# Kernel optimization log

Measured on AMD Instinct MI355X. Metric: run time of the kernel, lower is better.

The kernel has to match this reference:

```python
import jax, jax.numpy as jnp
import numpy as np

N = 100000
E = 1000000
N_FEAT = 128
N_HID = 16
N_HEAD = 8
HIDDEN = N_HID * N_HEAD  # 128
N_CLASS = 64
NEG_SLOPE = 0.2


def layer_norm(x, g, b, eps=1e-5):
    mu = x.mean(-1, keepdims=True)
    var = ((x - mu) ** 2).mean(-1, keepdims=True)
    return (x - mu) * jax.lax.rsqrt(var + eps) * g + b


def gat_conv(x, src, dst, W, a_src, a_dst, bias, concat):
    # Standard GATConv math (PyG): project, per-head additive attention,
    # softmax over incoming edges (self-loops included), weighted scatter-sum.
    H, C = a_src.shape
    n = x.shape[0]
    h = (x @ W).reshape(n, H, C)                      # [N,H,C]
    al = jnp.einsum('nhc,hc->nh', h, a_src)           # [N,H]
    ar = jnp.einsum('nhc,hc->nh', h, a_dst)
    e = jax.nn.leaky_relu(al[src] + ar[dst], NEG_SLOPE)  # [E',H]
    m = jax.ops.segment_max(e, dst, num_segments=n)
    m = jnp.where(jnp.isfinite(m), m, 0.0)
    ee = jnp.exp(e - m[dst])
    den = jax.ops.segment_sum(ee, dst, num_segments=n)
    alpha = ee / (den[dst] + 1e-16)                   # [E',H]
    out = jax.ops.segment_sum(h[src] * alpha[:, :, None], dst, num_segments=n)
    out = out.reshape(n, H * C) if concat else out.mean(1)
    return out + bias, h, alpha


def setup_inputs() -> dict:
    key = jax.random.key(0)
    ks = jax.random.split(key, 20)
    s = lambda *sh: 1.0 / np.sqrt(sh[-1])
    inp = {
        'x': jax.random.normal(ks[0], (N, N_FEAT), jnp.float32),
        'edge_index': jax.random.randint(ks[1], (2, E), 0, N, jnp.int32),
        # layer 1: n_feat -> n_hid x n_head (concat)
        'W1': jax.random.normal(ks[2], (N_FEAT, HIDDEN), jnp.float32) * s(N_FEAT),
        'a_src1': jax.random.normal(ks[3], (N_HEAD, N_HID), jnp.float32) * s(N_HID),
        'a_dst1': jax.random.normal(ks[4], (N_HEAD, N_HID), jnp.float32) * s(N_HID),
        'b1': jnp.zeros((HIDDEN,), jnp.float32),
        'g1': jnp.ones((HIDDEN,), jnp.float32),
        'be1': jnp.zeros((HIDDEN,), jnp.float32),
        # layer 2: hidden -> hidden (concat)
        'W2': jax.random.normal(ks[5], (HIDDEN, HIDDEN), jnp.float32) * s(HIDDEN),
        'a_src2': jax.random.normal(ks[6], (N_HEAD, N_HID), jnp.float32) * s(N_HID),
        'a_dst2': jax.random.normal(ks[7], (N_HEAD, N_HID), jnp.float32) * s(N_HID),
        'b2': jnp.zeros((HIDDEN,), jnp.float32),
        'g2': jnp.ones((HIDDEN,), jnp.float32),
        'be2': jnp.zeros((HIDDEN,), jnp.float32),
        # out layer: hidden -> n_class, 1 head, concat=False
        'W3': jax.random.normal(ks[8], (HIDDEN, N_CLASS), jnp.float32) * s(HIDDEN),
        'a_src3': jax.random.normal(ks[9], (1, N_CLASS), jnp.float32) * s(N_CLASS),
        'a_dst3': jax.random.normal(ks[10], (1, N_CLASS), jnp.float32) * s(N_CLASS),
        'b3': jnp.zeros((N_CLASS,), jnp.float32),
        'g3': jnp.ones((N_CLASS,), jnp.float32),
        'be3': jnp.zeros((N_CLASS,), jnp.float32),
    }
    return inp


def reference(x, edge_index, W1, a_src1, a_dst1, b1, g1, be1,
              W2, a_src2, a_dst2, b2, g2, be2,
              W3, a_src3, a_dst3, b3, g3, be3):
    # add self loops (GATConv default)
    loops = jnp.arange(N, dtype=edge_index.dtype)
    src = jnp.concatenate([edge_index[0], loops])
    dst = jnp.concatenate([edge_index[1], loops])
    # Transductive path, eval mode (dropout is identity)
    x, _, _ = gat_conv(x, src, dst, W1, a_src1, a_dst1, b1, concat=True)
    x = jax.nn.elu(layer_norm(x, g1, be1))
    x, _, _ = gat_conv(x, src, dst, W2, a_src2, a_dst2, b2, concat=True)
    x = jax.nn.elu(layer_norm(x, g2, be2))
    x, _, _ = gat_conv(x, src, dst, W3, a_src3, a_dst3, b3, concat=False)
    x = layer_norm(x, g3, be3)
    return x
```

## Files before the change

### kernel.cpp

```cpp
#include <hip/hip_runtime.h>
#include <math.h>

#define N_NODES 100000
#define N_EDGES 1000000
#define EP_EDGES (N_EDGES + N_NODES)
#define NBKT ((N_NODES + 255) / 256)
#define PAD 48

typedef short bf16x8 __attribute__((ext_vector_type(8)));
typedef float f32x4 __attribute__((ext_vector_type(4)));


__device__ inline unsigned bf16pack(float a, float b) {
    unsigned ua = __float_as_uint(a);
    unsigned ub = __float_as_uint(b);
    ua += 0x7FFFu + ((ua >> 16) & 1u);
    ub += 0x7FFFu + ((ub >> 16) & 1u);
    return (ua >> 16) | (ub & 0xFFFF0000u);
}

__device__ inline unsigned short bf16r(float a) {
    unsigned u = __float_as_uint(a);
    u += 0x7FFFu + ((u >> 16) & 1u);
    return (unsigned short)(u >> 16);
}

__device__ inline float bf16f(unsigned short v) {
    return __uint_as_float(((unsigned)v) << 16);
}

__device__ inline int swz(int o) { return o ^ (((o >> 8) & 7) << 4); }


__global__ void bkt_count(const int* __restrict__ ei, int* __restrict__ bktCnt) {
    __shared__ int hist[NBKT];
    int tid = threadIdx.x;
    for (int j = tid; j < NBKT; j += 256) hist[j] = 0;
    __syncthreads();
    int e0 = blockIdx.x * 4096;
    int e1 = min(e0 + 4096, EP_EDGES);
    for (int e = e0 + tid; e < e1; e += 256) {
        int d = (e < N_EDGES) ? ei[N_EDGES + e] : (e - N_EDGES);
        atomicAdd(&hist[d >> 8], 1);
    }
    __syncthreads();
    for (int j = tid; j < NBKT; j += 256) {
        int c = hist[j];
        if (c) atomicAdd(&bktCnt[j], c);
    }
}

__global__ void bkt_scan(const int* __restrict__ bktCnt, int* __restrict__ bktBase,
                         int* __restrict__ bktCursor) {
    __shared__ int tmp[512];
    int tid = threadIdx.x;
    int v = (tid < NBKT) ? bktCnt[tid] : 0;
    tmp[tid] = v;
    __syncthreads();
    int run = v;
    for (int off = 1; off < 512; off <<= 1) {
        int add = (tid >= off) ? tmp[tid - off] : 0;
        __syncthreads();
        run += add;
        tmp[tid] = run;
        __syncthreads();
    }
    if (tid <= NBKT) {
        int base = run - v;
        bktBase[tid] = base;
        if (tid < NBKT) bktCursor[tid] = base;
    }
}

__global__ void bkt_scatter(const int* __restrict__ ei, int* __restrict__ bktCursor,
                            unsigned* __restrict__ bktEdges) {
    __shared__ int hist[NBKT], chunk[NBKT];
    int tid = threadIdx.x;
    for (int j = tid; j < NBKT; j += 256) hist[j] = 0;
    __syncthreads();
    int e0 = blockIdx.x * 2048;
    int e1 = min(e0 + 2048, EP_EDGES);
    for (int e = e0 + tid; e < e1; e += 256) {
        int d = (e < N_EDGES) ? ei[N_EDGES + e] : (e - N_EDGES);
        atomicAdd(&hist[d >> 8], 1);
    }
    __syncthreads();
    for (int j = tid; j < NBKT; j += 256) {
        int c = hist[j];
        chunk[j] = c ? atomicAdd(&bktCursor[j], c) : 0;
        hist[j] = 0;
    }
    __syncthreads();
    for (int e = e0 + tid; e < e1; e += 256) {
        int s, d;
        if (e < N_EDGES) { s = ei[e]; d = ei[N_EDGES + e]; }
        else             { s = d = e - N_EDGES; }
        int b = d >> 8;
        int off = atomicAdd(&hist[b], 1);
        bktEdges[chunk[b] + off] = (unsigned)s | ((unsigned)(d & 255) << 24);
    }
}

__global__ void bkt_final(const unsigned* __restrict__ bktEdges, const int* __restrict__ bktBase,
                          int* __restrict__ deg_arr, int* __restrict__ pad_src) {
    __shared__ int hist[256], cur[256];
    int tid = threadIdx.x;
    int b = blockIdx.x;
    int base = bktBase[b], end = bktBase[b + 1];
    hist[tid] = 0;
    cur[tid] = 0;
    __syncthreads();
    for (int i = base + tid; i < end; i += 256)
        atomicAdd(&hist[bktEdges[i] >> 24], 1);
    __syncthreads();
    int node = b * 256 + tid;
    if (node < N_NODES) deg_arr[node] = min(hist[tid], PAD);
    __syncthreads();
    for (int i = base + tid; i < end; i += 256) {
        unsigned u = bktEdges[i];
        int d = u >> 24;
        int pos = atomicAdd(&cur[d], 1);
        if (pos < PAD)
            pad_src[(size_t)(b * 256 + d) * PAD + pos] = (int)(u & 0xFFFFFFu);
    }
    __syncthreads();
    for (int idx = tid; idx < 256 * PAD; idx += 256) {
        int dloc = idx / PAD, j = idx % PAD;
        int nd = b * 256 + dloc;
        if (nd < N_NODES && j >= min(hist[dloc], PAD))
            pad_src[(size_t)nd * PAD + j] = nd;
    }
}


__global__ void wt_prep_all(const float* __restrict__ W1, const float* __restrict__ W2,
                            const float* __restrict__ W3, unsigned short* __restrict__ Wt1,
                            unsigned short* __restrict__ Wt2, unsigned short* __restrict__ Wt3) {
    int t = blockIdx.x * 256 + threadIdx.x;
    if (t < 128 * 128) {
        int k = t >> 7, c = t & 127;
        Wt1[c * 128 + k] = bf16r(W1[t]);
        Wt2[c * 128 + k] = bf16r(W2[t]);
    }
    int t3 = t - 128 * 128;
    if (t3 >= 0 && t3 < 128 * 64) {
        int k = t3 >> 6, c = t3 & 63;
        Wt3[c * 128 + k] = bf16r(W3[t3]);
    }
}


template <int COUT, int H, bool IN_F32>
__launch_bounds__(256)
__global__ void gemm_mfma(const void* __restrict__ Xv, const unsigned short* __restrict__ Wt,
                          const float* __restrict__ a_src, const float* __restrict__ a_dst,
                          unsigned* __restrict__ hb16, unsigned short* __restrict__ alb,
                          float* __restrict__ ar, int n) {
    constexpr int NT = COUT / 16;
    __shared__ unsigned char lds[16384 + COUT * 256 + 1024];
    unsigned char* sx = lds;
    unsigned char* sw = lds + 16384;
    float* sc = (float*)sw;

    int tid = threadIdx.x;
    int row0 = blockIdx.x * 64;
    int lane = tid & 63;
    int wv = tid >> 6;

    if (IN_F32) {
        const float* Xf = (const float*)Xv;
        for (int c = tid; c < 1024; c += 256) {
            int o = c * 16;
            int row = o >> 8;
            int k0 = (o & 255) >> 1;
            int gr = row0 + row;
            float4 f0 = make_float4(0.f, 0.f, 0.f, 0.f), f1 = f0;
            if (gr < n) {
                f0 = *(const float4*)(Xf + (size_t)gr * 128 + k0);
                f1 = *(const float4*)(Xf + (size_t)gr * 128 + k0 + 4);
            }
            *(uint4*)(sx + swz(o)) = make_uint4(bf16pack(f0.x, f0.y), bf16pack(f0.z, f0.w),
                                                bf16pack(f1.x, f1.y), bf16pack(f1.z, f1.w));
        }
    } else {
        const unsigned char* Xb = (const unsigned char*)Xv;
        for (int c = tid; c < 1024; c += 256) {
            int o = c * 16;
            int row = o >> 8;
            int gr = row0 + row;
            uint4 v = make_uint4(0u, 0u, 0u, 0u);
            if (gr < n) v = *(const uint4*)(Xb + (size_t)gr * 256 + (o & 255));
            *(uint4*)(sx + swz(o)) = v;
        }
    }
    for (int c = tid; c < COUT * 16; c += 256) {
        int o = c * 16;
        *(uint4*)(sw + swz(o)) = *(const uint4*)((const unsigned char*)Wt + o);
    }
    __syncthreads();

    f32x4 acc[NT];
#pragma unroll
    for (int t = 0; t < NT; ++t) acc[t] = (f32x4){0.f, 0.f, 0.f, 0.f};
    int arow = wv * 16 + (lane & 15);
    int kg = lane >> 4;
#pragma unroll
    for (int s = 0; s < 4; ++s) {
        int ko = s * 64 + kg * 16;
        bf16x8 a = *(const bf16x8*)(sx + swz(arow * 256 + ko));
#pragma unroll
        for (int t = 0; t < NT; ++t) {
            bf16x8 bfr = *(const bf16x8*)(sw + swz((t * 16 + (lane & 15)) * 256 + ko));
            acc[t] = __builtin_amdgcn_mfma_f32_16x16x32_bf16(a, bfr, acc[t], 0, 0, 0);
        }
    }
    __syncthreads();

#pragma unroll
    for (int t = 0; t < NT; ++t)
#pragma unroll
        for (int i = 0; i < 4; ++i)
            sc[(wv * 16 + kg * 4 + i) * (COUT + 4) + t * 16 + (lane & 15)] = acc[t][i];
    __syncthreads();

    constexpr int NCG = COUT / 8;
    constexpr int ROWS = 64 * NCG / 256;
    int tc = tid % NCG, tr = tid / NCG;
    float asv[8], adv[8];
#pragma unroll
    for (int j = 0; j < 8; ++j) {
        asv[j] = a_src[tc * 8 + j];
        adv[j] = a_dst[tc * 8 + j];
    }
#pragma unroll
    for (int i = 0; i < ROWS; ++i) {
        int row = tr * ROWS + i;
        int gr = row0 + row;
        float h8[8];
        *(float4*)&h8[0] = *(const float4*)(sc + row * (COUT + 4) + tc * 8);
        *(float4*)&h8[4] = *(const float4*)(sc + row * (COUT + 4) + tc * 8 + 4);
        float pa = 0.f, pb = 0.f;
#pragma unroll
        for (int j = 0; j < 8; ++j) {
            pa = fmaf(h8[j], asv[j], pa);
            pb = fmaf(h8[j], adv[j], pb);
        }
        if (COUT / H == 16) {
            pa += __shfl_xor(pa, 1);
            pb += __shfl_xor(pb, 1);
            if ((tc & 1) == 0 && gr < n) {
                alb[gr * H + (tc >> 1)] = bf16r(pa);
                ar[gr * H + (tc >> 1)] = pb;
            }
        } else {
            pa += __shfl_xor(pa, 1); pb += __shfl_xor(pb, 1);
            pa += __shfl_xor(pa, 2); pb += __shfl_xor(pb, 2);
            pa += __shfl_xor(pa, 4); pb += __shfl_xor(pb, 4);
            if (tc == 0 && gr < n) {
                alb[gr] = bf16r(pa);
                ar[gr] = pb;
            }
        }
        if (gr < n) {
            *(uint4*)(hb16 + (size_t)gr * (COUT / 2) + tc * 4) =
                make_uint4(bf16pack(h8[0], h8[1]), bf16pack(h8[2], h8[3]),
                           bf16pack(h8[4], h8[5]), bf16pack(h8[6], h8[7]));
        }
    }
}


template <int H, int COUT, bool DO_ELU, bool OUTBF>
__launch_bounds__(256)
__global__ void gat_fused(const unsigned* __restrict__ hb16, const unsigned short* __restrict__ alb,
                          const float* __restrict__ ar, const int* __restrict__ deg_arr,
                          const int* __restrict__ pad_src, const float* __restrict__ bias,
                          const float* __restrict__ gamma, const float* __restrict__ beta,
                          void* __restrict__ outx, int n) {
    constexpr bool PAIR = (COUT == 128);
    __shared__ float wbuf[4][128];
    int node = blockIdx.x * 4 + (threadIdx.x >> 6);
    node = __builtin_amdgcn_readfirstlane(node);
    int l = threadIdx.x & 63;
    int wv = threadIdx.x >> 6;
    if (node >= n) return;

    int deg = deg_arr[node];
    const int* sp = pad_src + (size_t)node * PAD;
    const unsigned short* hbs = (const unsigned short*)hb16;

    int c0 = PAIR ? 2 * l : l;
    float bias0 = bias[c0], gam0 = gamma[c0], bet0 = beta[c0];
    float bias1 = 0.f, gam1 = 0.f, bet1 = 0.f;
    if (PAIR) { bias1 = bias[c0 + 1]; gam1 = gamma[c0 + 1]; bet1 = beta[c0 + 1]; }

    float acc0 = 0.f, acc1 = 0.f, den = 0.f;

    if (PAIR) {
        int eh = l & 7;
        int ej = l >> 3;
        int hc = l >> 3;
        float ar_e = ar[node * 8 + eh];
        bool hi = deg > 8;

        int s_lo = sp[ej];
        float a_lo = bf16f(alb[s_lo * 8 + eh]);
        unsigned rv_lo[8];
#pragma unroll
        for (int j = 0; j < 8; ++j) {
            int sj = __builtin_amdgcn_readlane(s_lo, j * 8);
            rv_lo[j] = hb16[(size_t)sj * 64 + l];
        }
        float e0 = a_lo + ar_e; e0 = (e0 >= 0.f) ? e0 : 0.2f * e0;
        float w_lo = (ej < deg) ? __expf(e0) : 0.f;
        float w_hi = 0.f;
        unsigned rv_hi[8];
        if (hi) {
            int s_hi = sp[8 + ej];
            float a_hi = bf16f(alb[s_hi * 8 + eh]);
#pragma unroll
            for (int j = 0; j < 8; ++j) {
                int sj = __builtin_amdgcn_readlane(s_hi, j * 8);
                rv_hi[j] = hb16[(size_t)sj * 64 + l];
            }
            float e1 = a_hi + ar_e; e1 = (e1 >= 0.f) ? e1 : 0.2f * e1;
            w_hi = (8 + ej < deg) ? __expf(e1) : 0.f;
        }

        *(float2*)&wbuf[wv][2 * l] = make_float2(w_lo, w_hi);
#pragma unroll
        for (int j = 0; j < 8; ++j) {
            float2 wj = *(const float2*)&wbuf[wv][2 * (j * 8 + hc)];
            den += wj.x + wj.y;
            acc0 = fmaf(wj.x, __uint_as_float(rv_lo[j] << 16), acc0);
            acc1 = fmaf(wj.x, __uint_as_float(rv_lo[j] & 0xFFFF0000u), acc1);
            if (hi) {
                acc0 = fmaf(wj.y, __uint_as_float(rv_hi[j] << 16), acc0);
                acc1 = fmaf(wj.y, __uint_as_float(rv_hi[j] & 0xFFFF0000u), acc1);
            }
        }

        for (int k = 16; k < deg; k += 8) {
            int s_c = sp[k + ej];
            float a = bf16f(alb[s_c * 8 + eh]);
            float e = a + ar_e; e = (e >= 0.f) ? e : 0.2f * e;
            float w = (k + ej < deg) ? __expf(e) : 0.f;
            unsigned rv[8];
#pragma unroll
            for (int j = 0; j < 8; ++j) {
                int sj = __builtin_amdgcn_readlane(s_c, j * 8);
                rv[j] = hb16[(size_t)sj * 64 + l];
            }
#pragma unroll
            for (int j = 0; j < 8; ++j) {
                float wj = __shfl(w, j * 8 + hc);
                den += wj;
                acc0 = fmaf(wj, __uint_as_float(rv[j] << 16), acc0);
                acc1 = fmaf(wj, __uint_as_float(rv[j] & 0xFFFF0000u), acc1);
            }
        }
    } else {
        float ar_e = ar[node];
        int idx = l < PAD ? l : PAD - 1;
        int s_cur = sp[idx];
        float a = bf16f(alb[s_cur]);
        float e = a + ar_e; e = (e >= 0.f) ? e : 0.2f * e;
        float w = (l < deg) ? __expf(e) : 0.f;
        int nsub = (deg + 7) >> 3;
        for (int sub = 0; sub < nsub; ++sub) {
            unsigned short rv[8];
#pragma unroll
            for (int j2 = 0; j2 < 8; ++j2) {
                int sj = __builtin_amdgcn_readlane(s_cur, sub * 8 + j2);
                rv[j2] = hbs[(size_t)sj * 64 + l];
            }
#pragma unroll
            for (int j2 = 0; j2 < 8; ++j2) {
                float wj = __uint_as_float(
                    __builtin_amdgcn_readlane(__float_as_uint(w), sub * 8 + j2));
                den += wj;
                acc0 = fmaf(wj, __uint_as_float(((unsigned)rv[j2]) << 16), acc0);
            }
        }
    }

    float inv = 1.f / (den + 1e-16f);
    float v0 = acc0 * inv + bias0;
    float v1 = 0.f;
    float ssum = v0;
    if (PAIR) { v1 = acc1 * inv + bias1; ssum += v1; }
    for (int off = 1; off < 64; off <<= 1) ssum += __shfl_xor(ssum, off);
    float mean = ssum / COUT;
    float d0 = v0 - mean, d1 = v1 - mean;
    float vs = PAIR ? (d0 * d0 + d1 * d1) : d0 * d0;
    for (int off = 1; off < 64; off <<= 1) vs += __shfl_xor(vs, off);
    float rstd = rsqrtf(vs / COUT + 1e-5f);
    float y0 = d0 * rstd * gam0 + bet0;
    if (DO_ELU) y0 = (y0 > 0.f) ? y0 : (__expf(y0) - 1.f);
    if (PAIR) {
        float y1 = d1 * rstd * gam1 + bet1;
        if (DO_ELU) y1 = (y1 > 0.f) ? y1 : (__expf(y1) - 1.f);
        if (OUTBF) {
            ((unsigned*)outx)[(size_t)node * 64 + l] = bf16pack(y0, y1);
        } else {
            *(float2*)((float*)outx + (size_t)node * COUT + c0) = make_float2(y0, y1);
        }
    } else {
        ((float*)outx)[(size_t)node * COUT + c0] = y0;
    }
}


extern "C" void kernel_launch(void* const* d_in, const int* in_sizes, int n_in,
                              void* d_out, int out_size, void* d_ws, size_t ws_size,
                              hipStream_t stream) {
    const float* x   = (const float*)d_in[0];
    const int*   ei  = (const int*)d_in[1];
    const float* W1  = (const float*)d_in[2];
    const float* as1 = (const float*)d_in[3];
    const float* ad1 = (const float*)d_in[4];
    const float* b1  = (const float*)d_in[5];
    const float* g1  = (const float*)d_in[6];
    const float* be1 = (const float*)d_in[7];
    const float* W2  = (const float*)d_in[8];
    const float* as2 = (const float*)d_in[9];
    const float* ad2 = (const float*)d_in[10];
    const float* b2  = (const float*)d_in[11];
    const float* g2  = (const float*)d_in[12];
    const float* be2 = (const float*)d_in[13];
    const float* W3  = (const float*)d_in[14];
    const float* as3 = (const float*)d_in[15];
    const float* ad3 = (const float*)d_in[16];
    const float* b3  = (const float*)d_in[17];
    const float* g3  = (const float*)d_in[18];
    const float* be3 = (const float*)d_in[19];
    float* out = (float*)d_out;

    char* p = (char*)d_ws;
    auto alloc = [&](size_t bytes) -> char* {
        char* r = p;
        p += (bytes + 255) & ~size_t(255);
        return r;
    };
    unsigned* hb16   = (unsigned*)alloc((size_t)N_NODES * 64 * 4);
    unsigned* xbuf   = (unsigned*)alloc((size_t)N_NODES * 64 * 4);
    unsigned short* alb = (unsigned short*)alloc((size_t)N_NODES * 8 * 2);
    float* ar        = (float*)alloc((size_t)N_NODES * 8 * 4);
    int*   deg_arr   = (int*)alloc((size_t)N_NODES * 4);
    int*   pad_src   = (int*)alloc((size_t)N_NODES * PAD * 4);
    unsigned* bktEdges = (unsigned*)alloc((size_t)EP_EDGES * 4);
    int*   bktCnt    = (int*)alloc((size_t)(NBKT + 1) * 4);
    int*   bktBase   = (int*)alloc((size_t)(NBKT + 1) * 4);
    int*   bktCursor = (int*)alloc((size_t)(NBKT + 1) * 4);
    unsigned short* Wt1 = (unsigned short*)alloc((size_t)128 * 128 * 2);
    unsigned short* Wt2 = (unsigned short*)alloc((size_t)128 * 128 * 2);
    unsigned short* Wt3 = (unsigned short*)alloc((size_t)64 * 128 * 2);

    hipMemsetAsync(bktCnt, 0, (size_t)(NBKT + 1) * 4, stream);

    wt_prep_all<<<(128 * 128 + 128 * 64 + 255) / 256, 256, 0, stream>>>(W1, W2, W3,
                                                                        Wt1, Wt2, Wt3);

    bkt_count<<<(EP_EDGES + 4095) / 4096, 256, 0, stream>>>(ei, bktCnt);
    bkt_scan<<<1, 512, 0, stream>>>(bktCnt, bktBase, bktCursor);
    bkt_scatter<<<(EP_EDGES + 2047) / 2048, 256, 0, stream>>>(ei, bktCursor, bktEdges);
    bkt_final<<<NBKT, 256, 0, stream>>>(bktEdges, bktBase, deg_arr, pad_src);

    const int gemm_grid = (N_NODES + 63) / 64;
    const int agg_grid  = (N_NODES + 3) / 4;

    gemm_mfma<128, 8, true><<<gemm_grid, 256, 0, stream>>>(x, Wt1, as1, ad1,
                                                           hb16, alb, ar, N_NODES);
    gat_fused<8, 128, true, true><<<agg_grid, 256, 0, stream>>>(hb16, alb, ar, deg_arr, pad_src,
                                                                b1, g1, be1, xbuf, N_NODES);
    gemm_mfma<128, 8, false><<<gemm_grid, 256, 0, stream>>>(xbuf, Wt2, as2, ad2,
                                                            hb16, alb, ar, N_NODES);
    gat_fused<8, 128, true, true><<<agg_grid, 256, 0, stream>>>(hb16, alb, ar, deg_arr, pad_src,
                                                                b2, g2, be2, xbuf, N_NODES);
    gemm_mfma<64, 1, false><<<gemm_grid, 256, 0, stream>>>(xbuf, Wt3, as3, ad3,
                                                           hb16, alb, ar, N_NODES);
    gat_fused<1, 64, false, false><<<agg_grid, 256, 0, stream>>>(hb16, alb, ar, deg_arr, pad_src,
                                                                 b3, g3, be3, out, N_NODES);
}
```

Before: 262.7 us.

## Merge weight prep into bucket count, trim aggregation address math and denominator work

Weight transposition is folded into the bucket-count kernel as extra blocks, which removes one launch. In the aggregation kernel, gathers now use 32-bit byte-offset addressing instead of size_t indexing. The per-edge denominator accumulation is replaced by a per-lane partial sum followed by a shuffle reduction. The high-half bf16 mask is dropped, so the low bits of each packed word are left in the mantissa, a small numeric deviation. Bias, gamma and beta loads are also vectorised and deferred past the edge loop to ease register pressure.

```diff
diff --git a/kernel.cpp b/kernel.cpp
--- a/kernel.cpp
+++ b/kernel.cpp
@@ -6,6 +6,8 @@
 #define EP_EDGES (N_EDGES + N_NODES)
 #define NBKT ((N_NODES + 255) / 256)
 #define PAD 48
+#define NB_COUNT ((EP_EDGES + 4095) / 4096)
+#define NB_WT ((128 * 128 + 128 * 64 + 255) / 256)
 
 typedef short bf16x8 __attribute__((ext_vector_type(8)));
 typedef float f32x4 __attribute__((ext_vector_type(4)));
@@ -32,21 +34,39 @@
 __device__ inline int swz(int o) { return o ^ (((o >> 8) & 7) << 4); }
 
 
-__global__ void bkt_count(const int* __restrict__ ei, int* __restrict__ bktCnt) {
+__global__ void prep_count(const int* __restrict__ ei, int* __restrict__ bktCnt,
+                           const float* __restrict__ W1, const float* __restrict__ W2,
+                           const float* __restrict__ W3, unsigned short* __restrict__ Wt1,
+                           unsigned short* __restrict__ Wt2, unsigned short* __restrict__ Wt3) {
     __shared__ int hist[NBKT];
     int tid = threadIdx.x;
-    for (int j = tid; j < NBKT; j += 256) hist[j] = 0;
-    __syncthreads();
-    int e0 = blockIdx.x * 4096;
-    int e1 = min(e0 + 4096, EP_EDGES);
-    for (int e = e0 + tid; e < e1; e += 256) {
-        int d = (e < N_EDGES) ? ei[N_EDGES + e] : (e - N_EDGES);
-        atomicAdd(&hist[d >> 8], 1);
-    }
-    __syncthreads();
-    for (int j = tid; j < NBKT; j += 256) {
-        int c = hist[j];
-        if (c) atomicAdd(&bktCnt[j], c);
+    int b = blockIdx.x;
+    if (b < NB_COUNT) {
+        for (int j = tid; j < NBKT; j += 256) hist[j] = 0;
+        __syncthreads();
+        int e0 = b * 4096;
+        int e1 = min(e0 + 4096, EP_EDGES);
+        for (int e = e0 + tid; e < e1; e += 256) {
+            int d = (e < N_EDGES) ? ei[N_EDGES + e] : (e - N_EDGES);
+            atomicAdd(&hist[d >> 8], 1);
+        }
+        __syncthreads();
+        for (int j = tid; j < NBKT; j += 256) {
+            int c = hist[j];
+            if (c) atomicAdd(&bktCnt[j], c);
+        }
+    } else {
+        int t = (b - NB_COUNT) * 256 + tid;
+        if (t < 128 * 128) {
+            int k = t >> 7, c = t & 127;
+            Wt1[c * 128 + k] = bf16r(W1[t]);
+            Wt2[c * 128 + k] = bf16r(W2[t]);
+        }
+        int t3 = t - 128 * 128;
+        if (t3 >= 0 && t3 < 128 * 64) {
+            int k = t3 >> 6, c = t3 & 63;
+            Wt3[c * 128 + k] = bf16r(W3[t3]);
+        }
     }
 }
 
@@ -129,23 +149,6 @@
         int nd = b * 256 + dloc;
         if (nd < N_NODES && j >= min(hist[dloc], PAD))
             pad_src[(size_t)nd * PAD + j] = nd;
-    }
-}
-
-
-__global__ void wt_prep_all(const float* __restrict__ W1, const float* __restrict__ W2,
-                            const float* __restrict__ W3, unsigned short* __restrict__ Wt1,
-                            unsigned short* __restrict__ Wt2, unsigned short* __restrict__ Wt3) {
-    int t = blockIdx.x * 256 + threadIdx.x;
-    if (t < 128 * 128) {
-        int k = t >> 7, c = t & 127;
-        Wt1[c * 128 + k] = bf16r(W1[t]);
-        Wt2[c * 128 + k] = bf16r(W2[t]);
-    }
-    int t3 = t - 128 * 128;
-    if (t3 >= 0 && t3 < 128 * 64) {
-        int k = t3 >> 6, c = t3 & 63;
-        Wt3[c * 128 + k] = bf16r(W3[t3]);
     }
 }
 
@@ -287,16 +290,14 @@
 
     int deg = deg_arr[node];
     const int* sp = pad_src + (size_t)node * PAD;
-    const unsigned short* hbs = (const unsigned short*)hb16;
-
+    const unsigned char* hbB = (const unsigned char*)hb16;
+    const unsigned char* albB = (const unsigned char*)alb;
+
+    float acc0 = 0.f, acc1 = 0.f, den;
     int c0 = PAIR ? 2 * l : l;
-    float bias0 = bias[c0], gam0 = gamma[c0], bet0 = beta[c0];
-    float bias1 = 0.f, gam1 = 0.f, bet1 = 0.f;
-    if (PAIR) { bias1 = bias[c0 + 1]; gam1 = gamma[c0 + 1]; bet1 = beta[c0 + 1]; }
-
-    float acc0 = 0.f, acc1 = 0.f, den = 0.f;
 
     if (PAIR) {
+        unsigned loff = (unsigned)l * 4u;
         int eh = l & 7;
         int ej = l >> 3;
         int hc = l >> 3;
@@ -304,12 +305,12 @@
         bool hi = deg > 8;
 
         int s_lo = sp[ej];
-        float a_lo = bf16f(alb[s_lo * 8 + eh]);
+        float a_lo = bf16f(*(const unsigned short*)(albB + (((unsigned)s_lo) << 4) + ((unsigned)eh << 1)));
         unsigned rv_lo[8];
 #pragma unroll
         for (int j = 0; j < 8; ++j) {
             int sj = __builtin_amdgcn_readlane(s_lo, j * 8);
-            rv_lo[j] = hb16[(size_t)sj * 64 + l];
+            rv_lo[j] = *(const unsigned*)(hbB + (((unsigned)sj) << 8) + loff);
         }
         float e0 = a_lo + ar_e; e0 = (e0 >= 0.f) ? e0 : 0.2f * e0;
         float w_lo = (ej < deg) ? __expf(e0) : 0.f;
@@ -317,88 +318,106 @@
         unsigned rv_hi[8];
         if (hi) {
             int s_hi = sp[8 + ej];
-            float a_hi = bf16f(alb[s_hi * 8 + eh]);
+            float a_hi = bf16f(*(const unsigned short*)(albB + (((unsigned)s_hi) << 4) + ((unsigned)eh << 1)));
 #pragma unroll
             for (int j = 0; j < 8; ++j) {
                 int sj = __builtin_amdgcn_readlane(s_hi, j * 8);
-                rv_hi[j] = hb16[(size_t)sj * 64 + l];
+                rv_hi[j] = *(const unsigned*)(hbB + (((unsigned)sj) << 8) + loff);
             }
             float e1 = a_hi + ar_e; e1 = (e1 >= 0.f) ? e1 : 0.2f * e1;
             w_hi = (8 + ej < deg) ? __expf(e1) : 0.f;
         }
+        float den_bf = w_lo + w_hi;
 
         *(float2*)&wbuf[wv][2 * l] = make_float2(w_lo, w_hi);
 #pragma unroll
         for (int j = 0; j < 8; ++j) {
             float2 wj = *(const float2*)&wbuf[wv][2 * (j * 8 + hc)];
-            den += wj.x + wj.y;
             acc0 = fmaf(wj.x, __uint_as_float(rv_lo[j] << 16), acc0);
-            acc1 = fmaf(wj.x, __uint_as_float(rv_lo[j] & 0xFFFF0000u), acc1);
+            acc1 = fmaf(wj.x, __uint_as_float(rv_lo[j]), acc1);
             if (hi) {
                 acc0 = fmaf(wj.y, __uint_as_float(rv_hi[j] << 16), acc0);
-                acc1 = fmaf(wj.y, __uint_as_float(rv_hi[j] & 0xFFFF0000u), acc1);
+                acc1 = fmaf(wj.y, __uint_as_float(rv_hi[j]), acc1);
             }
         }
 
         for (int k = 16; k < deg; k += 8) {
             int s_c = sp[k + ej];
-            float a = bf16f(alb[s_c * 8 + eh]);
+            float a = bf16f(*(const unsigned short*)(albB + (((unsigned)s_c) << 4) + ((unsigned)eh << 1)));
             float e = a + ar_e; e = (e >= 0.f) ? e : 0.2f * e;
             float w = (k + ej < deg) ? __expf(e) : 0.f;
+            den_bf += w;
             unsigned rv[8];
 #pragma unroll
             for (int j = 0; j < 8; ++j) {
                 int sj = __builtin_amdgcn_readlane(s_c, j * 8);
-                rv[j] = hb16[(size_t)sj * 64 + l];
+                rv[j] = *(const unsigned*)(hbB + (((unsigned)sj) << 8) + loff);
             }
 #pragma unroll
             for (int j = 0; j < 8; ++j) {
                 float wj = __shfl(w, j * 8 + hc);
-                den += wj;
                 acc0 = fmaf(wj, __uint_as_float(rv[j] << 16), acc0);
-                acc1 = fmaf(wj, __uint_as_float(rv[j] & 0xFFFF0000u), acc1);
-            }
-        }
+                acc1 = fmaf(wj, __uint_as_float(rv[j]), acc1);
+            }
+        }
+
+        den_bf += __shfl_xor(den_bf, 8);
+        den_bf += __shfl_xor(den_bf, 16);
+        den_bf += __shfl_xor(den_bf, 32);
+        den = __shfl(den_bf, hc);
     } else {
+        unsigned loff2 = (unsigned)l * 2u;
         float ar_e = ar[node];
-        int idx = l < PAD ? l : PAD - 1;
-        int s_cur = sp[idx];
-        float a = bf16f(alb[s_cur]);
+        int slot = (l < PAD) ? l : 0;
+        int s_cur = sp[slot];
+        float a = bf16f(*(const unsigned short*)(albB + ((unsigned)s_cur << 1)));
         float e = a + ar_e; e = (e >= 0.f) ? e : 0.2f * e;
         float w = (l < deg) ? __expf(e) : 0.f;
+        float den_bf = w;
+        den_bf += __shfl_xor(den_bf, 1);
+        den_bf += __shfl_xor(den_bf, 2);
+        den_bf += __shfl_xor(den_bf, 4);
+        den_bf += __shfl_xor(den_bf, 8);
+        den_bf += __shfl_xor(den_bf, 16);
+        den_bf += __shfl_xor(den_bf, 32);
+        den = den_bf;
         int nsub = (deg + 7) >> 3;
         for (int sub = 0; sub < nsub; ++sub) {
-            unsigned short rv[8];
 #pragma unroll
             for (int j2 = 0; j2 < 8; ++j2) {
-                int sj = __builtin_amdgcn_readlane(s_cur, sub * 8 + j2);
-                rv[j2] = hbs[(size_t)sj * 64 + l];
-            }
-#pragma unroll
-            for (int j2 = 0; j2 < 8; ++j2) {
-                float wj = __uint_as_float(
-                    __builtin_amdgcn_readlane(__float_as_uint(w), sub * 8 + j2));
-                den += wj;
-                acc0 = fmaf(wj, __uint_as_float(((unsigned)rv[j2]) << 16), acc0);
-            }
-        }
-    }
-
+                int lidx = sub * 8 + j2;
+                int sj = __builtin_amdgcn_readlane(s_cur, lidx);
+                float wj = __uint_as_float(__builtin_amdgcn_readlane(__float_as_uint(w), lidx));
+                unsigned short rvs = *(const unsigned short*)(hbB + (((unsigned)sj) << 7) + loff2);
+                acc0 = fmaf(wj, __uint_as_float(((unsigned)rvs) << 16), acc0);
+            }
+        }
+    }
+
+    float b0, b1v = 0.f, g0, g1v = 0.f, t0, t1v = 0.f;
+    if (PAIR) {
+        float2 bb = *(const float2*)(bias + c0);
+        float2 gg = *(const float2*)(gamma + c0);
+        float2 tt = *(const float2*)(beta + c0);
+        b0 = bb.x; b1v = bb.y; g0 = gg.x; g1v = gg.y; t0 = tt.x; t1v = tt.y;
+    } else {
+        b0 = bias[c0]; g0 = gamma[c0]; t0 = beta[c0];
+    }
     float inv = 1.f / (den + 1e-16f);
-    float v0 = acc0 * inv + bias0;
+    float v0 = acc0 * inv + b0;
     float v1 = 0.f;
     float ssum = v0;
-    if (PAIR) { v1 = acc1 * inv + bias1; ssum += v1; }
+    if (PAIR) { v1 = acc1 * inv + b1v; ssum += v1; }
     for (int off = 1; off < 64; off <<= 1) ssum += __shfl_xor(ssum, off);
     float mean = ssum / COUT;
     float d0 = v0 - mean, d1 = v1 - mean;
     float vs = PAIR ? (d0 * d0 + d1 * d1) : d0 * d0;
     for (int off = 1; off < 64; off <<= 1) vs += __shfl_xor(vs, off);
     float rstd = rsqrtf(vs / COUT + 1e-5f);
-    float y0 = d0 * rstd * gam0 + bet0;
+    float y0 = d0 * rstd * g0 + t0;
     if (DO_ELU) y0 = (y0 > 0.f) ? y0 : (__expf(y0) - 1.f);
     if (PAIR) {
-        float y1 = d1 * rstd * gam1 + bet1;
+        float y1 = d1 * rstd * g1v + t1v;
         if (DO_ELU) y1 = (y1 > 0.f) ? y1 : (__expf(y1) - 1.f);
         if (OUTBF) {
             ((unsigned*)outx)[(size_t)node * 64 + l] = bf16pack(y0, y1);
@@ -458,10 +477,7 @@
 
     hipMemsetAsync(bktCnt, 0, (size_t)(NBKT + 1) * 4, stream);
 
-    wt_prep_all<<<(128 * 128 + 128 * 64 + 255) / 256, 256, 0, stream>>>(W1, W2, W3,
-                                                                        Wt1, Wt2, Wt3);
-
-    bkt_count<<<(EP_EDGES + 4095) / 4096, 256, 0, stream>>>(ei, bktCnt);
+    prep_count<<<NB_COUNT + NB_WT, 256, 0, stream>>>(ei, bktCnt, W1, W2, W3, Wt1, Wt2, Wt3);
     bkt_scan<<<1, 512, 0, stream>>>(bktCnt, bktBase, bktCursor);
     bkt_scatter<<<(EP_EDGES + 2047) / 2048, 256, 0, stream>>>(ei, bktCursor, bktEdges);
     bkt_final<<<NBKT, 256, 0, stream>>>(bktEdges, bktBase, deg_arr, pad_src);
```

Result: no change. 262.2 us (-0.2%).
